# Kernel tuning notes

Measured on AMD Instinct MI355X. Metric: run time of the kernel, lower is better.

The kernel has to match this reference:

```python
import jax, jax.numpy as jnp
import numpy as np

EPS = 1e-12  # torch F.normalize default eps


def _l2_normalize(t):
    n = jnp.linalg.norm(t, axis=-1, keepdims=True)
    return t / jnp.maximum(n, EPS)


def _block(x, W, alpha):
    # x: [B,H,N,D]; W: [D,D] (torch Linear weight, applied as x @ W.T)
    xn = _l2_normalize(x)                                   # q_norm == k_norm (q=k=x)
    A = jnp.einsum('bhnd,bhmd->bhnm', xn, xn)               # cosine similarity [B,H,N,N]
    A = jax.nn.softmax(A / jnp.maximum(alpha, 0.01), axis=-1)
    av = jnp.einsum('bhnm,bhmd->bhnd', A, x)                # A @ v, v = x
    return jax.nn.relu(jnp.einsum('bhnd,ed->bhne', av, W) + x)


def setup_inputs() -> dict:
    key = jax.random.key(0)
    k1, k2, k3 = jax.random.split(key, 3)
    B, H, N, D = 4, 4, 4096, 64
    x = jax.random.normal(k1, (B, H, N, D), dtype=jnp.float32)
    # nn.Linear(dim, dim, bias=False) weights, kaiming-uniform-ish scale
    bound = 1.0 / np.sqrt(D)
    W1 = jax.random.uniform(k2, (D, D), dtype=jnp.float32, minval=-bound, maxval=bound)
    W2 = jax.random.uniform(k3, (D, D), dtype=jnp.float32, minval=-bound, maxval=bound)
    alpha1 = jnp.float32(1.0)
    alpha2 = jnp.float32(1.0)
    return {"x": x, "W1": W1, "W2": W2, "alpha1": alpha1, "alpha2": alpha2}


def reference(x, W1, W2, alpha1, alpha2):
    x = _block(x, W1, alpha1)
    x = _block(x, W2, alpha2)
    return x
```

## Files before the change

kernel.cpp:

```cpp
#include <hip/hip_runtime.h>

typedef unsigned short u16;
typedef unsigned int   u32;
typedef __bf16 bf16x8 __attribute__((ext_vector_type(8)));
typedef float  f32x16 __attribute__((ext_vector_type(16)));

#define BH    16
#define NSEQ  4096
#define DIM   64
#define BM    128
#define BN    64
#define LDP   72
#define NTH   32
#define QTILES (NSEQ / BM)

#define SK_OFF   0
#define SV_OFF   9216
#define SW_OFF   18432
#define LX_OFF   23040
#define SMEM_U16 23552
#define HBUF     4608

__device__ __forceinline__ float bf2f(u16 u) {
    union { u32 i; float f; } v; v.i = ((u32)u) << 16; return v.f;
}
__device__ __forceinline__ u16 f2bf(float f) {
    union { float f; u32 i; } v; v.f = f;
    u32 r = v.i + 0x7fffu + ((v.i >> 16) & 1u);
    return (u16)(r >> 16);
}
#if __has_builtin(__builtin_amdgcn_exp2f)
__device__ __forceinline__ float exp2_raw(float x) { return __builtin_amdgcn_exp2f(x); }
#else
__device__ __forceinline__ float exp2_raw(float x) {
    float r; asm("v_exp_f32 %0, %1" : "=v"(r) : "v"(x)); return r;
}
#endif
__device__ __forceinline__ u32 cvtpk(float a, float b) {
    u32 r; asm("v_cvt_pk_bf16_f32 %0, %1, %2" : "=v"(r) : "v"(a), "v"(b)); return r;
}
__device__ __forceinline__ void plswap(u32& a, u32& b) {
    asm("v_permlane32_swap_b32 %0, %1" : "+v"(a), "+v"(b));
}
__device__ __forceinline__ void lds_barrier() {
    asm volatile("s_waitcnt lgkmcnt(0)\n\ts_barrier" ::: "memory");
}

__global__ __launch_bounds__(256) void ContentGCN_5059471475267_prep(
    const void* __restrict__ src, int isf,
    u16* __restrict__ xn, u16* __restrict__ xT)
{
    __shared__ u16 tile[64 * 72];
    int bh = blockIdx.x >> 6, nt = blockIdx.x & 63, tid = threadIdx.x;
    int r = tid >> 2, cg = (tid & 3) * 16;
    size_t base = ((size_t)bh * NSEQ + nt * 64 + r) * DIM + cg;

    float v[16];
    if (isf) {
        const float4* g = (const float4*)((const float*)src + base);
#pragma unroll
        for (int i = 0; i < 4; i++) {
            float4 t = g[i];
            v[4*i] = t.x; v[4*i+1] = t.y; v[4*i+2] = t.z; v[4*i+3] = t.w;
        }
    } else {
        alignas(16) u16 tmp[16];
        const uint4* g = (const uint4*)((const u16*)src + base);
        ((uint4*)tmp)[0] = g[0]; ((uint4*)tmp)[1] = g[1];
#pragma unroll
        for (int d = 0; d < 16; d++) v[d] = bf2f(tmp[d]);
    }

    float ss = 0.f;
#pragma unroll
    for (int d = 0; d < 16; d++) ss += v[d] * v[d];
    ss += __shfl_xor(ss, 1);
    ss += __shfl_xor(ss, 2);
    float n = sqrtf(ss);
    if (n < 1e-12f) n = 1e-12f;
    float inv = 1.0f / n;

    alignas(16) u16 nb[16], rb[16];
#pragma unroll
    for (int d = 0; d < 16; d++) { nb[d] = f2bf(v[d] * inv); rb[d] = f2bf(v[d]); }
    uint4* gn = (uint4*)(xn + base);
    gn[0] = ((uint4*)nb)[0]; gn[1] = ((uint4*)nb)[1];

    uint4* tr = (uint4*)&tile[r * 72 + cg];
    tr[0] = ((uint4*)rb)[0]; tr[1] = ((uint4*)rb)[1];
    __syncthreads();

    int d = tid >> 2, sc = (tid & 3) * 16;
    alignas(16) u16 ob[16];
#pragma unroll
    for (int j = 0; j < 16; j++) ob[j] = tile[(sc + j) * 72 + d];
    uint4* gt = (uint4*)(xT + ((size_t)bh * DIM + d) * NSEQ + (size_t)nt * 64 + sc);
    gt[0] = ((uint4*)ob)[0]; gt[1] = ((uint4*)ob)[1];
}

__global__ __launch_bounds__(512, 4) void ContentGCN_5059471475267_attn(
    const u16* __restrict__ xn, const u16* __restrict__ xT,
    const void* __restrict__ res, int res_isf,
    const float* __restrict__ Wt, const float* __restrict__ alphap,
    void* __restrict__ outp, int out_isf)
{
    __shared__ u16 smem[SMEM_U16];
    u16* sK = smem + SK_OFF;
    u16* sV = smem + SV_OFF;
    u16* sW = smem + SW_OFF;
    float* lX = (float*)(smem + LX_OFF);

    int tid  = threadIdx.x;
    int w    = tid >> 6, lane = tid & 63;
    int half = w >> 2,  wv   = w & 3;
    int l31  = lane & 31, hi = lane >> 5;
    int bh   = blockIdx.x >> 5;
    int qt   = blockIdx.x & 31;

    float scale = 1.4426950408889634f / fmaxf(alphap[0], 0.01f);

    {
        int rr = tid >> 3, c0 = (tid & 7) * 8;
        const float4* gw = (const float4*)(Wt + rr * DIM + c0);
        float4 t0 = gw[0], t1 = gw[1];
        alignas(16) u16 wb[8];
        wb[0] = f2bf(t0.x); wb[1] = f2bf(t0.y); wb[2] = f2bf(t0.z); wb[3] = f2bf(t0.w);
        wb[4] = f2bf(t1.x); wb[5] = f2bf(t1.y); wb[6] = f2bf(t1.z); wb[7] = f2bf(t1.w);
        *(uint4*)&sW[rr * LDP + c0] = *(const uint4*)wb;
    }

    int qrow = qt * BM + wv * 32 + l31;
    const u16* qp = xn + ((size_t)bh * NSEQ + qrow) * DIM + hi * 8;
    bf16x8 bQ0 = *(const bf16x8*)(qp);
    bf16x8 bQ1 = *(const bf16x8*)(qp + 16);
    bf16x8 bQ2 = *(const bf16x8*)(qp + 32);
    bf16x8 bQ3 = *(const bf16x8*)(qp + 48);

    f32x16 z16;
#pragma unroll
    for (int i = 0; i < 16; i++) z16[i] = 0.f;
    f32x16 OT0 = z16, OT1 = z16;
    float la0 = 0.f, la1 = 0.f, la2 = 0.f, la3 = 0.f;

    u16* sKh = sK + half * HBUF;
    u16* sVh = sV + half * HBUF;

    int ltid = tid & 255;
    int srow = ltid >> 2, scol = (ltid & 3) * 16;

    const u16* pk = xn + ((size_t)bh * NSEQ + half * (NTH * BN) + srow) * DIM + scol;
    const u16* pv = xT + ((size_t)bh * DIM + srow) * NSEQ + half * (NTH * BN) + scol;
    uint4 ck0 = ((const uint4*)pk)[0], ck1 = ((const uint4*)pk)[1];
    uint4 cv0 = ((const uint4*)pv)[0], cv1 = ((const uint4*)pv)[1];
    pk += (size_t)BN * DIM; pv += BN;

    const u16* kB = sKh + l31 * LDP + hi * 8;
    const u16* vB0 = sVh + l31 * LDP + hi * 8;
    const u16* vB1 = sVh + (32 + l31) * LDP + hi * 8;

    for (int kt = 0; kt < NTH; kt++) {
        lds_barrier();
        *(uint4*)&sKh[srow * LDP + scol]     = ck0;
        *(uint4*)&sKh[srow * LDP + scol + 8] = ck1;
        *(uint4*)&sVh[srow * LDP + scol]     = cv0;
        *(uint4*)&sVh[srow * LDP + scol + 8] = cv1;
        if (kt + 1 < NTH) {
            ck0 = ((const uint4*)pk)[0]; ck1 = ((const uint4*)pk)[1];
            cv0 = ((const uint4*)pv)[0]; cv1 = ((const uint4*)pv)[1];
            pk += (size_t)BN * DIM; pv += BN;
        }
        lds_barrier();

#pragma unroll
        for (int kb = 0; kb < 2; kb++) {
            const u16* kb0 = kB + kb * 32 * LDP;
            f32x16 ST;
            ST = __builtin_amdgcn_mfma_f32_32x32x16_bf16(*(const bf16x8*)(kb0),      bQ0, z16, 0, 0, 0);
            ST = __builtin_amdgcn_mfma_f32_32x32x16_bf16(*(const bf16x8*)(kb0 + 16), bQ1, ST,  0, 0, 0);
            ST = __builtin_amdgcn_mfma_f32_32x32x16_bf16(*(const bf16x8*)(kb0 + 32), bQ2, ST,  0, 0, 0);
            ST = __builtin_amdgcn_mfma_f32_32x32x16_bf16(*(const bf16x8*)(kb0 + 48), bQ3, ST,  0, 0, 0);

            float p0  = exp2_raw(fmaf(ST[0],  scale, -scale));
            float p1  = exp2_raw(fmaf(ST[1],  scale, -scale));
            float p2  = exp2_raw(fmaf(ST[2],  scale, -scale));
            float p3  = exp2_raw(fmaf(ST[3],  scale, -scale));
            float p4  = exp2_raw(fmaf(ST[4],  scale, -scale));
            float p5  = exp2_raw(fmaf(ST[5],  scale, -scale));
            float p6  = exp2_raw(fmaf(ST[6],  scale, -scale));
            float p7  = exp2_raw(fmaf(ST[7],  scale, -scale));
            float p8  = exp2_raw(fmaf(ST[8],  scale, -scale));
            float p9  = exp2_raw(fmaf(ST[9],  scale, -scale));
            float p10 = exp2_raw(fmaf(ST[10], scale, -scale));
            float p11 = exp2_raw(fmaf(ST[11], scale, -scale));
            float p12 = exp2_raw(fmaf(ST[12], scale, -scale));
            float p13 = exp2_raw(fmaf(ST[13], scale, -scale));
            float p14 = exp2_raw(fmaf(ST[14], scale, -scale));
            float p15 = exp2_raw(fmaf(ST[15], scale, -scale));

            la0 += (p0 + p4) + (p8  + p12);
            la1 += (p1 + p5) + (p9  + p13);
            la2 += (p2 + p6) + (p10 + p14);
            la3 += (p3 + p7) + (p11 + p15);

            u32 w0 = cvtpk(p0,  p1),  w1 = cvtpk(p2,  p3);
            u32 w2 = cvtpk(p4,  p5),  w3 = cvtpk(p6,  p7);
            u32 w4 = cvtpk(p8,  p9),  w5 = cvtpk(p10, p11);
            u32 w6 = cvtpk(p12, p13), w7 = cvtpk(p14, p15);
            plswap(w0, w2); plswap(w1, w3);
            plswap(w4, w6); plswap(w5, w7);
            union { u32 u[4]; bf16x8 v; } bp0, bp1;
            bp0.u[0] = w0; bp0.u[1] = w1; bp0.u[2] = w2; bp0.u[3] = w3;
            bp1.u[0] = w4; bp1.u[1] = w5; bp1.u[2] = w6; bp1.u[3] = w7;

            const u16* v0 = vB0 + kb * 32;
            const u16* v1 = vB1 + kb * 32;
            OT0 = __builtin_amdgcn_mfma_f32_32x32x16_bf16(*(const bf16x8*)(v0),      bp0.v, OT0, 0, 0, 0);
            OT0 = __builtin_amdgcn_mfma_f32_32x32x16_bf16(*(const bf16x8*)(v0 + 16), bp1.v, OT0, 0, 0, 0);
            OT1 = __builtin_amdgcn_mfma_f32_32x32x16_bf16(*(const bf16x8*)(v1),      bp0.v, OT1, 0, 0, 0);
            OT1 = __builtin_amdgcn_mfma_f32_32x32x16_bf16(*(const bf16x8*)(v1 + 16), bp1.v, OT1, 0, 0, 0);
        }
    }

    float lsum = (la0 + la1) + (la2 + la3);
    u32 ja = __float_as_uint(lsum), jb = ja;
    plswap(ja, jb);
    float lfull = __uint_as_float(ja) + __uint_as_float(jb);

    __syncthreads();
    if (lane < 32) lX[w * 32 + l31] = lfull;
    __syncthreads();
    float invl = 1.0f / (lfull + lX[(w ^ 4) * 32 + l31]);

    union { u32 u[4]; bf16x8 v; } av0, av1, av2, av3;
    {
        u32 x0 = cvtpk(OT0[0]  * invl, OT0[1]  * invl), x1 = cvtpk(OT0[2]  * invl, OT0[3]  * invl);
        u32 x2 = cvtpk(OT0[4]  * invl, OT0[5]  * invl), x3 = cvtpk(OT0[6]  * invl, OT0[7]  * invl);
        u32 x4 = cvtpk(OT0[8]  * invl, OT0[9]  * invl), x5 = cvtpk(OT0[10] * invl, OT0[11] * invl);
        u32 x6 = cvtpk(OT0[12] * invl, OT0[13] * invl), x7 = cvtpk(OT0[14] * invl, OT0[15] * invl);
        plswap(x0, x2); plswap(x1, x3); plswap(x4, x6); plswap(x5, x7);
        av0.u[0] = x0; av0.u[1] = x1; av0.u[2] = x2; av0.u[3] = x3;
        av1.u[0] = x4; av1.u[1] = x5; av1.u[2] = x6; av1.u[3] = x7;
        u32 y0 = cvtpk(OT1[0]  * invl, OT1[1]  * invl), y1 = cvtpk(OT1[2]  * invl, OT1[3]  * invl);
        u32 y2 = cvtpk(OT1[4]  * invl, OT1[5]  * invl), y3 = cvtpk(OT1[6]  * invl, OT1[7]  * invl);
        u32 y4 = cvtpk(OT1[8]  * invl, OT1[9]  * invl), y5 = cvtpk(OT1[10] * invl, OT1[11] * invl);
        u32 y6 = cvtpk(OT1[12] * invl, OT1[13] * invl), y7 = cvtpk(OT1[14] * invl, OT1[15] * invl);
        plswap(y0, y2); plswap(y1, y3); plswap(y4, y6); plswap(y5, y7);
        av2.u[0] = y0; av2.u[1] = y1; av2.u[2] = y2; av2.u[3] = y3;
        av3.u[0] = y4; av3.u[1] = y5; av3.u[2] = y6; av3.u[3] = y7;
    }

    f32x16 R0, R1;
    {
        const u16* w0p = sW + l31 * LDP + hi * 8;
        const u16* w1p = sW + (32 + l31) * LDP + hi * 8;
        R0 = __builtin_amdgcn_mfma_f32_32x32x16_bf16(*(const bf16x8*)(w0p),      av0.v, z16, 0, 0, 0);
        R0 = __builtin_amdgcn_mfma_f32_32x32x16_bf16(*(const bf16x8*)(w0p + 16), av1.v, R0,  0, 0, 0);
        R0 = __builtin_amdgcn_mfma_f32_32x32x16_bf16(*(const bf16x8*)(w0p + 32), av2.v, R0,  0, 0, 0);
        R0 = __builtin_amdgcn_mfma_f32_32x32x16_bf16(*(const bf16x8*)(w0p + 48), av3.v, R0,  0, 0, 0);
        R1 = __builtin_amdgcn_mfma_f32_32x32x16_bf16(*(const bf16x8*)(w1p),      av0.v, z16, 0, 0, 0);
        R1 = __builtin_amdgcn_mfma_f32_32x32x16_bf16(*(const bf16x8*)(w1p + 16), av1.v, R1,  0, 0, 0);
        R1 = __builtin_amdgcn_mfma_f32_32x32x16_bf16(*(const bf16x8*)(w1p + 32), av2.v, R1,  0, 0, 0);
        R1 = __builtin_amdgcn_mfma_f32_32x32x16_bf16(*(const bf16x8*)(w1p + 48), av3.v, R1,  0, 0, 0);
    }

    float* outS = (float*)smem;
    if (half == 0) {
#pragma unroll
        for (int r = 0; r < 16; r++) {
            int e0 = (r & 3) + 8 * (r >> 2) + 4 * hi;
            outS[e0 * 133 + wv * 32 + l31]        = R0[r];
            outS[(e0 + 32) * 133 + wv * 32 + l31] = R1[r];
        }
    }
    __syncthreads();
    if (half == 1) {
#pragma unroll
        for (int r = 0; r < 16; r++) {
            int e0 = (r & 3) + 8 * (r >> 2) + 4 * hi;
            outS[e0 * 133 + wv * 32 + l31]        += R0[r];
            outS[(e0 + 32) * 133 + wv * 32 + l31] += R1[r];
        }
    }
    __syncthreads();

    {
        int q = tid >> 2, c = tid & 3;
        size_t gbase = ((size_t)bh * NSEQ + qt * BM + q) * DIM + c * 16;
        float vv[16];
#pragma unroll
        for (int j = 0; j < 16; j++) vv[j] = outS[(c * 16 + j) * 133 + q];
        if (res_isf) {
            const float4* rp = (const float4*)((const float*)res + gbase);
#pragma unroll
            for (int i = 0; i < 4; i++) {
                float4 t = rp[i];
                vv[4*i] += t.x; vv[4*i+1] += t.y; vv[4*i+2] += t.z; vv[4*i+3] += t.w;
            }
        } else {
            alignas(16) u16 rb[16];
            const uint4* rp = (const uint4*)((const u16*)res + gbase);
            ((uint4*)rb)[0] = rp[0]; ((uint4*)rb)[1] = rp[1];
#pragma unroll
            for (int j = 0; j < 16; j++) vv[j] += bf2f(rb[j]);
        }
#pragma unroll
        for (int j = 0; j < 16; j++) vv[j] = (vv[j] < 0.f) ? 0.f : vv[j];
        if (out_isf) {
            float4* op = (float4*)((float*)outp + gbase);
#pragma unroll
            for (int i = 0; i < 4; i++)
                op[i] = make_float4(vv[4*i], vv[4*i+1], vv[4*i+2], vv[4*i+3]);
        } else {
            alignas(16) u16 ob[16];
#pragma unroll
            for (int j = 0; j < 16; j++) ob[j] = f2bf(vv[j]);
            uint4* op = (uint4*)((u16*)outp + gbase);
            op[0] = ((uint4*)ob)[0]; op[1] = ((uint4*)ob)[1];
        }
    }
}

extern "C" void kernel_launch(void* const* d_in, const int* in_sizes, int n_in,
                              void* d_out, int out_size, void* d_ws, size_t ws_size,
                              hipStream_t stream) {
    const float* x  = (const float*)d_in[0];
    const float* W1 = (const float*)d_in[1];
    const float* W2 = (const float*)d_in[2];
    const float* a1 = (const float*)d_in[3];
    const float* a2 = (const float*)d_in[4];
    float* outp = (float*)d_out;

    size_t elems = (size_t)BH * NSEQ * DIM;
    u16* xn = (u16*)d_ws;
    u16* xT = xn + elems;
    u16* y1 = xT + elems;

    dim3 pgrid(BH * 64),     pblk(256);
    dim3 agrid(BH * QTILES), ablk(512);

    ContentGCN_5059471475267_prep<<<pgrid, pblk, 0, stream>>>(x, 1, xn, xT);
    ContentGCN_5059471475267_attn<<<agrid, ablk, 0, stream>>>(xn, xT, x, 1, W1, a1, y1, 0);
    ContentGCN_5059471475267_prep<<<pgrid, pblk, 0, stream>>>(y1, 0, xn, xT);
    ContentGCN_5059471475267_attn<<<agrid, ablk, 0, stream>>>(xn, xT, y1, 0, W2, a2, outp, 1);
}
```

Baseline: 248.0 us.

## Use LDS transpose reads for V and fuse second-block normalization into attention epilogue

V is now kept row-major (no transposed copy), staged into LDS in a swizzled layout and read with ds_read_b64_tr_b16 so the MFMA operand is transposed on load. The first attention kernel's epilogue now also writes the L2-normalized bf16 output, which removes the second prep launch and its global round trip. This adds inline asm with explicit waitcnt and sched barriers that may limit overlap, and it depends on the transpose-read layout math being correct.

```diff
diff --git a/kernel.cpp b/kernel.cpp
--- a/kernel.cpp
+++ b/kernel.cpp
@@ -4,6 +4,7 @@
 typedef unsigned int   u32;
 typedef __bf16 bf16x8 __attribute__((ext_vector_type(8)));
 typedef float  f32x16 __attribute__((ext_vector_type(16)));
+typedef u32    u32x2  __attribute__((ext_vector_type(2)));
 
 #define BH    16
 #define NSEQ  4096
@@ -16,10 +17,13 @@
 
 #define SK_OFF   0
 #define SV_OFF   9216
-#define SW_OFF   18432
-#define LX_OFF   23040
-#define SMEM_U16 23552
-#define HBUF     4608
+#define SW_OFF   17408
+#define LX_OFF   22016
+#define SMEM_U16 22528
+#define K_HBUF   4608
+#define V_HBUF   4096
+
+#define MFMA __builtin_amdgcn_mfma_f32_32x32x16_bf16
 
 __device__ __forceinline__ float bf2f(u16 u) {
     union { u32 i; float f; } v; v.i = ((u32)u) << 16; return v.f;
@@ -47,28 +51,18 @@
 }
 
 __global__ __launch_bounds__(256) void ContentGCN_5059471475267_prep(
-    const void* __restrict__ src, int isf,
-    u16* __restrict__ xn, u16* __restrict__ xT)
+    const float* __restrict__ src, u16* __restrict__ xn, u16* __restrict__ xr)
 {
-    __shared__ u16 tile[64 * 72];
     int bh = blockIdx.x >> 6, nt = blockIdx.x & 63, tid = threadIdx.x;
     int r = tid >> 2, cg = (tid & 3) * 16;
     size_t base = ((size_t)bh * NSEQ + nt * 64 + r) * DIM + cg;
 
     float v[16];
-    if (isf) {
-        const float4* g = (const float4*)((const float*)src + base);
-#pragma unroll
-        for (int i = 0; i < 4; i++) {
-            float4 t = g[i];
-            v[4*i] = t.x; v[4*i+1] = t.y; v[4*i+2] = t.z; v[4*i+3] = t.w;
-        }
-    } else {
-        alignas(16) u16 tmp[16];
-        const uint4* g = (const uint4*)((const u16*)src + base);
-        ((uint4*)tmp)[0] = g[0]; ((uint4*)tmp)[1] = g[1];
-#pragma unroll
-        for (int d = 0; d < 16; d++) v[d] = bf2f(tmp[d]);
+    const float4* g = (const float4*)(src + base);
+#pragma unroll
+    for (int i = 0; i < 4; i++) {
+        float4 t = g[i];
+        v[4*i] = t.x; v[4*i+1] = t.y; v[4*i+2] = t.z; v[4*i+3] = t.w;
     }
 
     float ss = 0.f;
@@ -85,24 +79,15 @@
     for (int d = 0; d < 16; d++) { nb[d] = f2bf(v[d] * inv); rb[d] = f2bf(v[d]); }
     uint4* gn = (uint4*)(xn + base);
     gn[0] = ((uint4*)nb)[0]; gn[1] = ((uint4*)nb)[1];
-
-    uint4* tr = (uint4*)&tile[r * 72 + cg];
-    tr[0] = ((uint4*)rb)[0]; tr[1] = ((uint4*)rb)[1];
-    __syncthreads();
-
-    int d = tid >> 2, sc = (tid & 3) * 16;
-    alignas(16) u16 ob[16];
-#pragma unroll
-    for (int j = 0; j < 16; j++) ob[j] = tile[(sc + j) * 72 + d];
-    uint4* gt = (uint4*)(xT + ((size_t)bh * DIM + d) * NSEQ + (size_t)nt * 64 + sc);
-    gt[0] = ((uint4*)ob)[0]; gt[1] = ((uint4*)ob)[1];
+    uint4* gr = (uint4*)(xr + base);
+    gr[0] = ((uint4*)rb)[0]; gr[1] = ((uint4*)rb)[1];
 }
 
 __global__ __launch_bounds__(512, 4) void ContentGCN_5059471475267_attn(
-    const u16* __restrict__ xn, const u16* __restrict__ xT,
+    const u16* __restrict__ xn, const u16* __restrict__ xr,
     const void* __restrict__ res, int res_isf,
     const float* __restrict__ Wt, const float* __restrict__ alphap,
-    void* __restrict__ outp, int out_isf)
+    void* __restrict__ outp, int out_isf, u16* __restrict__ xnout)
 {
     __shared__ u16 smem[SMEM_U16];
     u16* sK = smem + SK_OFF;
@@ -142,84 +127,110 @@
     f32x16 OT0 = z16, OT1 = z16;
     float la0 = 0.f, la1 = 0.f, la2 = 0.f, la3 = 0.f;
 
-    u16* sKh = sK + half * HBUF;
-    u16* sVh = sV + half * HBUF;
+    u16* sKh = sK + half * K_HBUF;
+    u16* sVh = sV + half * V_HBUF;
 
     int ltid = tid & 255;
     int srow = ltid >> 2, scol = (ltid & 3) * 16;
+    int vsaddr = ((scol >> 4) * 16 + (srow >> 2)) * 64 + (srow & 3) * 16;
 
     const u16* pk = xn + ((size_t)bh * NSEQ + half * (NTH * BN) + srow) * DIM + scol;
-    const u16* pv = xT + ((size_t)bh * DIM + srow) * NSEQ + half * (NTH * BN) + scol;
+    const u16* pv = xr + ((size_t)bh * NSEQ + half * (NTH * BN) + srow) * DIM + scol;
     uint4 ck0 = ((const uint4*)pk)[0], ck1 = ((const uint4*)pk)[1];
     uint4 cv0 = ((const uint4*)pv)[0], cv1 = ((const uint4*)pv)[1];
-    pk += (size_t)BN * DIM; pv += BN;
+    pk += (size_t)BN * DIM; pv += (size_t)BN * DIM;
 
     const u16* kB = sKh + l31 * LDP + hi * 8;
-    const u16* vB0 = sVh + l31 * LDP + hi * 8;
-    const u16* vB1 = sVh + (32 + l31) * LDP + hi * 8;
+
+    u32 trbase = (u32)(uintptr_t)&sVh[0]
+               + ((u32)((lane >> 4) & 1)) * 2048u
+               + ((u32)hi) * 256u
+               + ((u32)(lane & 15)) * 8u;
+
+#define KBSTEP(KB)                                                              \
+    {                                                                           \
+        const u16* kb0 = kB + (KB) * 32 * LDP;                                  \
+        f32x16 ST;                                                              \
+        ST = MFMA(*(const bf16x8*)(kb0),      bQ0, z16, 0, 0, 0);               \
+        ST = MFMA(*(const bf16x8*)(kb0 + 16), bQ1, ST,  0, 0, 0);               \
+        ST = MFMA(*(const bf16x8*)(kb0 + 32), bQ2, ST,  0, 0, 0);               \
+        ST = MFMA(*(const bf16x8*)(kb0 + 48), bQ3, ST,  0, 0, 0);               \
+        u32x2 t00, t01, t10, t11, t20, t21, t30, t31;                           \
+        asm volatile("ds_read_b64_tr_b16 %0, %1 offset:%2"                      \
+            : "=&v"(t00) : "v"(trbase), "i"((((KB)*8 + 0) * 128)));             \
+        asm volatile("ds_read_b64_tr_b16 %0, %1 offset:%2"                      \
+            : "=&v"(t01) : "v"(trbase), "i"((((KB)*8 + 1) * 128)));             \
+        asm volatile("ds_read_b64_tr_b16 %0, %1 offset:%2"                      \
+            : "=&v"(t10) : "v"(trbase), "i"((((KB)*8 + 4) * 128)));             \
+        asm volatile("ds_read_b64_tr_b16 %0, %1 offset:%2"                      \
+            : "=&v"(t11) : "v"(trbase), "i"((((KB)*8 + 5) * 128)));             \
+        asm volatile("ds_read_b64_tr_b16 %0, %1 offset:%2"                      \
+            : "=&v"(t20) : "v"(trbase), "i"((4096 + ((KB)*8 + 0) * 128)));      \
+        asm volatile("ds_read_b64_tr_b16 %0, %1 offset:%2"                      \
+            : "=&v"(t21) : "v"(trbase), "i"((4096 + ((KB)*8 + 1) * 128)));      \
+        asm volatile("ds_read_b64_tr_b16 %0, %1 offset:%2"                      \
+            : "=&v"(t30) : "v"(trbase), "i"((4096 + ((KB)*8 + 4) * 128)));      \
+        asm volatile("ds_read_b64_tr_b16 %0, %1 offset:%2"                      \
+            : "=&v"(t31) : "v"(trbase), "i"((4096 + ((KB)*8 + 5) * 128)));      \
+        float p0  = exp2_raw(fmaf(ST[0],  scale, -scale));                      \
+        float p1  = exp2_raw(fmaf(ST[1],  scale, -scale));                      \
+        float p2  = exp2_raw(fmaf(ST[2],  scale, -scale));                      \
+        float p3  = exp2_raw(fmaf(ST[3],  scale, -scale));                      \
+        float p4  = exp2_raw(fmaf(ST[4],  scale, -scale));                      \
+        float p5  = exp2_raw(fmaf(ST[5],  scale, -scale));                      \
+        float p6  = exp2_raw(fmaf(ST[6],  scale, -scale));                      \
+        float p7  = exp2_raw(fmaf(ST[7],  scale, -scale));                      \
+        float p8  = exp2_raw(fmaf(ST[8],  scale, -scale));                      \
+        float p9  = exp2_raw(fmaf(ST[9],  scale, -scale));                      \
+        float p10 = exp2_raw(fmaf(ST[10], scale, -scale));                      \
+        float p11 = exp2_raw(fmaf(ST[11], scale, -scale));                      \
+        float p12 = exp2_raw(fmaf(ST[12], scale, -scale));                      \
+        float p13 = exp2_raw(fmaf(ST[13], scale, -scale));                      \
+        float p14 = exp2_raw(fmaf(ST[14], scale, -scale));                      \
+        float p15 = exp2_raw(fmaf(ST[15], scale, -scale));                      \
+        la0 += (p0 + p4) + (p8  + p12);                                         \
+        la1 += (p1 + p5) + (p9  + p13);                                         \
+        la2 += (p2 + p6) + (p10 + p14);                                         \
+        la3 += (p3 + p7) + (p11 + p15);                                         \
+        u32 w0 = cvtpk(p0,  p1),  w1 = cvtpk(p2,  p3);                          \
+        u32 w2 = cvtpk(p4,  p5),  w3 = cvtpk(p6,  p7);                          \
+        u32 w4 = cvtpk(p8,  p9),  w5 = cvtpk(p10, p11);                         \
+        u32 w6 = cvtpk(p12, p13), w7 = cvtpk(p14, p15);                         \
+        plswap(w0, w2); plswap(w1, w3);                                         \
+        plswap(w4, w6); plswap(w5, w7);                                         \
+        union { u32 u[4]; bf16x8 v; } bp0, bp1;                                 \
+        bp0.u[0] = w0; bp0.u[1] = w1; bp0.u[2] = w2; bp0.u[3] = w3;             \
+        bp1.u[0] = w4; bp1.u[1] = w5; bp1.u[2] = w6; bp1.u[3] = w7;             \
+        asm volatile("s_waitcnt lgkmcnt(0)" ::: "memory");                      \
+        __builtin_amdgcn_sched_barrier(0);                                      \
+        union { u32 u[4]; bf16x8 v; } vf00, vf01, vf10, vf11;                   \
+        vf00.u[0] = t00.x; vf00.u[1] = t00.y; vf00.u[2] = t01.x; vf00.u[3] = t01.y; \
+        vf01.u[0] = t10.x; vf01.u[1] = t10.y; vf01.u[2] = t11.x; vf01.u[3] = t11.y; \
+        vf10.u[0] = t20.x; vf10.u[1] = t20.y; vf10.u[2] = t21.x; vf10.u[3] = t21.y; \
+        vf11.u[0] = t30.x; vf11.u[1] = t30.y; vf11.u[2] = t31.x; vf11.u[3] = t31.y; \
+        OT0 = MFMA(vf00.v, bp0.v, OT0, 0, 0, 0);                                \
+        OT0 = MFMA(vf01.v, bp1.v, OT0, 0, 0, 0);                                \
+        OT1 = MFMA(vf10.v, bp0.v, OT1, 0, 0, 0);                                \
+        OT1 = MFMA(vf11.v, bp1.v, OT1, 0, 0, 0);                                \
+    }
 
     for (int kt = 0; kt < NTH; kt++) {
         lds_barrier();
         *(uint4*)&sKh[srow * LDP + scol]     = ck0;
         *(uint4*)&sKh[srow * LDP + scol + 8] = ck1;
-        *(uint4*)&sVh[srow * LDP + scol]     = cv0;
-        *(uint4*)&sVh[srow * LDP + scol + 8] = cv1;
+        *(uint4*)&sVh[vsaddr]     = cv0;
+        *(uint4*)&sVh[vsaddr + 8] = cv1;
         if (kt + 1 < NTH) {
             ck0 = ((const uint4*)pk)[0]; ck1 = ((const uint4*)pk)[1];
             cv0 = ((const uint4*)pv)[0]; cv1 = ((const uint4*)pv)[1];
-            pk += (size_t)BN * DIM; pv += BN;
+            pk += (size_t)BN * DIM; pv += (size_t)BN * DIM;
         }
         lds_barrier();
 
-#pragma unroll
-        for (int kb = 0; kb < 2; kb++) {
-            const u16* kb0 = kB + kb * 32 * LDP;
-            f32x16 ST;
-            ST = __builtin_amdgcn_mfma_f32_32x32x16_bf16(*(const bf16x8*)(kb0),      bQ0, z16, 0, 0, 0);
-            ST = __builtin_amdgcn_mfma_f32_32x32x16_bf16(*(const bf16x8*)(kb0 + 16), bQ1, ST,  0, 0, 0);
-            ST = __builtin_amdgcn_mfma_f32_32x32x16_bf16(*(const bf16x8*)(kb0 + 32), bQ2, ST,  0, 0, 0);
-            ST = __builtin_amdgcn_mfma_f32_32x32x16_bf16(*(const bf16x8*)(kb0 + 48), bQ3, ST,  0, 0, 0);
-
-            float p0  = exp2_raw(fmaf(ST[0],  scale, -scale));
-            float p1  = exp2_raw(fmaf(ST[1],  scale, -scale));
-            float p2  = exp2_raw(fmaf(ST[2],  scale, -scale));
-            float p3  = exp2_raw(fmaf(ST[3],  scale, -scale));
-            float p4  = exp2_raw(fmaf(ST[4],  scale, -scale));
-            float p5  = exp2_raw(fmaf(ST[5],  scale, -scale));
-            float p6  = exp2_raw(fmaf(ST[6],  scale, -scale));
-            float p7  = exp2_raw(fmaf(ST[7],  scale, -scale));
-            float p8  = exp2_raw(fmaf(ST[8],  scale, -scale));
-            float p9  = exp2_raw(fmaf(ST[9],  scale, -scale));
-            float p10 = exp2_raw(fmaf(ST[10], scale, -scale));
-            float p11 = exp2_raw(fmaf(ST[11], scale, -scale));
-            float p12 = exp2_raw(fmaf(ST[12], scale, -scale));
-            float p13 = exp2_raw(fmaf(ST[13], scale, -scale));
-            float p14 = exp2_raw(fmaf(ST[14], scale, -scale));
-            float p15 = exp2_raw(fmaf(ST[15], scale, -scale));
-
-            la0 += (p0 + p4) + (p8  + p12);
-            la1 += (p1 + p5) + (p9  + p13);
-            la2 += (p2 + p6) + (p10 + p14);
-            la3 += (p3 + p7) + (p11 + p15);
-
-            u32 w0 = cvtpk(p0,  p1),  w1 = cvtpk(p2,  p3);
-            u32 w2 = cvtpk(p4,  p5),  w3 = cvtpk(p6,  p7);
-            u32 w4 = cvtpk(p8,  p9),  w5 = cvtpk(p10, p11);
-            u32 w6 = cvtpk(p12, p13), w7 = cvtpk(p14, p15);
-            plswap(w0, w2); plswap(w1, w3);
-            plswap(w4, w6); plswap(w5, w7);
-            union { u32 u[4]; bf16x8 v; } bp0, bp1;
-            bp0.u[0] = w0; bp0.u[1] = w1; bp0.u[2] = w2; bp0.u[3] = w3;
-            bp1.u[0] = w4; bp1.u[1] = w5; bp1.u[2] = w6; bp1.u[3] = w7;
-
-            const u16* v0 = vB0 + kb * 32;
-            const u16* v1 = vB1 + kb * 32;
-            OT0 = __builtin_amdgcn_mfma_f32_32x32x16_bf16(*(const bf16x8*)(v0),      bp0.v, OT0, 0, 0, 0);
-            OT0 = __builtin_amdgcn_mfma_f32_32x32x16_bf16(*(const bf16x8*)(v0 + 16), bp1.v, OT0, 0, 0, 0);
-            OT1 = __builtin_amdgcn_mfma_f32_32x32x16_bf16(*(const bf16x8*)(v1),      bp0.v, OT1, 0, 0, 0);
-            OT1 = __builtin_amdgcn_mfma_f32_32x32x16_bf16(*(const bf16x8*)(v1 + 16), bp1.v, OT1, 0, 0, 0);
-        }
-    }
+        KBSTEP(0)
+        KBSTEP(1)
+    }
+#undef KBSTEP
 
     float lsum = (la0 + la1) + (la2 + la3);
     u32 ja = __float_as_uint(lsum), jb = ja;
@@ -253,14 +264,14 @@
     {
         const u16* w0p = sW + l31 * LDP + hi * 8;
         const u16* w1p = sW + (32 + l31) * LDP + hi * 8;
-        R0 = __builtin_amdgcn_mfma_f32_32x32x16_bf16(*(const bf16x8*)(w0p),      av0.v, z16, 0, 0, 0);
-        R0 = __builtin_amdgcn_mfma_f32_32x32x16_bf16(*(const bf16x8*)(w0p + 16), av1.v, R0,  0, 0, 0);
-        R0 = __builtin_amdgcn_mfma_f32_32x32x16_bf16(*(const bf16x8*)(w0p + 32), av2.v, R0,  0, 0, 0);
-        R0 = __builtin_amdgcn_mfma_f32_32x32x16_bf16(*(const bf16x8*)(w0p + 48), av3.v, R0,  0, 0, 0);
-        R1 = __builtin_amdgcn_mfma_f32_32x32x16_bf16(*(const bf16x8*)(w1p),      av0.v, z16, 0, 0, 0);
-        R1 = __builtin_amdgcn_mfma_f32_32x32x16_bf16(*(const bf16x8*)(w1p + 16), av1.v, R1,  0, 0, 0);
-        R1 = __builtin_amdgcn_mfma_f32_32x32x16_bf16(*(const bf16x8*)(w1p + 32), av2.v, R1,  0, 0, 0);
-        R1 = __builtin_amdgcn_mfma_f32_32x32x16_bf16(*(const bf16x8*)(w1p + 48), av3.v, R1,  0, 0, 0);
+        R0 = MFMA(*(const bf16x8*)(w0p),      av0.v, z16, 0, 0, 0);
+        R0 = MFMA(*(const bf16x8*)(w0p + 16), av1.v, R0,  0, 0, 0);
+        R0 = MFMA(*(const bf16x8*)(w0p + 32), av2.v, R0,  0, 0, 0);
+        R0 = MFMA(*(const bf16x8*)(w0p + 48), av3.v, R0,  0, 0, 0);
+        R1 = MFMA(*(const bf16x8*)(w1p),      av0.v, z16, 0, 0, 0);
+        R1 = MFMA(*(const bf16x8*)(w1p + 16), av1.v, R1,  0, 0, 0);
+        R1 = MFMA(*(const bf16x8*)(w1p + 32), av2.v, R1,  0, 0, 0);
+        R1 = MFMA(*(const bf16x8*)(w1p + 48), av3.v, R1,  0, 0, 0);
     }
 
     float* outS = (float*)smem;
@@ -316,6 +327,21 @@
             for (int j = 0; j < 16; j++) ob[j] = f2bf(vv[j]);
             uint4* op = (uint4*)((u16*)outp + gbase);
             op[0] = ((uint4*)ob)[0]; op[1] = ((uint4*)ob)[1];
+        }
+        if (xnout) {
+            float ss = 0.f;
+#pragma unroll
+            for (int j = 0; j < 16; j++) ss += vv[j] * vv[j];
+            ss += __shfl_xor(ss, 1);
+            ss += __shfl_xor(ss, 2);
+            float n = sqrtf(ss);
+            if (n < 1e-12f) n = 1e-12f;
+            float inv = 1.0f / n;
+            alignas(16) u16 nb[16];
+#pragma unroll
+            for (int j = 0; j < 16; j++) nb[j] = f2bf(vv[j] * inv);
+            uint4* gn = (uint4*)(xnout + gbase);
+            gn[0] = ((uint4*)nb)[0]; gn[1] = ((uint4*)nb)[1];
         }
     }
 }
@@ -331,15 +357,17 @@
     float* outp = (float*)d_out;
 
     size_t elems = (size_t)BH * NSEQ * DIM;
-    u16* xn = (u16*)d_ws;
-    u16* xT = xn + elems;
-    u16* y1 = xT + elems;
+    u16* xn1 = (u16*)d_ws;
+    u16* xr1 = xn1 + elems;
+    u16* xn2 = xr1 + elems;
+    u16* xr2 = xn2 + elems;
 
     dim3 pgrid(BH * 64),     pblk(256);
     dim3 agrid(BH * QTILES), ablk(512);
 
-    ContentGCN_5059471475267_prep<<<pgrid, pblk, 0, stream>>>(x, 1, xn, xT);
-    ContentGCN_5059471475267_attn<<<agrid, ablk, 0, stream>>>(xn, xT, x, 1, W1, a1, y1, 0);
-    ContentGCN_5059471475267_prep<<<pgrid, pblk, 0, stream>>>(y1, 0, xn, xT);
-    ContentGCN_5059471475267_attn<<<agrid, ablk, 0, stream>>>(xn, xT, y1, 0, W2, a2, outp, 1);
-}
+    ContentGCN_5059471475267_prep<<<pgrid, pblk, 0, stream>>>(x, xn1, xr1);
+    ContentGCN_5059471475267_attn<<<agrid, ablk, 0, stream>>>(
+        xn1, xr1, x, 1, W1, a1, xr2, 0, xn2);
+    ContentGCN_5059471475267_attn<<<agrid, ablk, 0, stream>>>(
+        xn2, xr2, xr2, 0, W2, a2, outp, 1, nullptr);
+}
```

Result: slower. 272.7 us (+9.9%).

## Fuse second-block normalization into attn epilogue and restructure QK/PV MFMA schedule

Applied to the files above, without the earlier changes.

The first attention kernel's epilogue now also L2-normalizes its output rows and writes them as bf16 to a new buffer. The second prep pass therefore only has to transpose y1, and the prep kernels now give each thread a full row, with 256 rows per block. The inner loop issues both QK^T MFMA chains before the exp/PV work and wraps the MFMA groups in s_setprio so matrix work can overlap with the exp computation. The cost is higher register pressure (64-float rows in prep, two score accumulators in attn) and extra epilogue work in the attention kernel.

```diff
diff --git a/kernel.cpp b/kernel.cpp
--- a/kernel.cpp
+++ b/kernel.cpp
@@ -21,6 +21,8 @@
 #define SMEM_U16 23552
 #define HBUF     4608
 
+#define MFMA __builtin_amdgcn_mfma_f32_32x32x16_bf16
+
 __device__ __forceinline__ float bf2f(u16 u) {
     union { u32 i; float f; } v; v.i = ((u32)u) << 16; return v.f;
 }
@@ -47,62 +49,75 @@
 }
 
 __global__ __launch_bounds__(256) void ContentGCN_5059471475267_prep(
-    const void* __restrict__ src, int isf,
-    u16* __restrict__ xn, u16* __restrict__ xT)
+    const float* __restrict__ src, u16* __restrict__ xn, u16* __restrict__ xT)
 {
-    __shared__ u16 tile[64 * 72];
-    int bh = blockIdx.x >> 6, nt = blockIdx.x & 63, tid = threadIdx.x;
-    int r = tid >> 2, cg = (tid & 3) * 16;
-    size_t base = ((size_t)bh * NSEQ + nt * 64 + r) * DIM + cg;
-
-    float v[16];
-    if (isf) {
-        const float4* g = (const float4*)((const float*)src + base);
-#pragma unroll
-        for (int i = 0; i < 4; i++) {
-            float4 t = g[i];
-            v[4*i] = t.x; v[4*i+1] = t.y; v[4*i+2] = t.z; v[4*i+3] = t.w;
-        }
-    } else {
-        alignas(16) u16 tmp[16];
-        const uint4* g = (const uint4*)((const u16*)src + base);
-        ((uint4*)tmp)[0] = g[0]; ((uint4*)tmp)[1] = g[1];
-#pragma unroll
-        for (int d = 0; d < 16; d++) v[d] = bf2f(tmp[d]);
+    __shared__ u16 tile[256 * 72];
+    int bh = blockIdx.x >> 4, nt = blockIdx.x & 15, tid = threadIdx.x;
+    size_t base = ((size_t)bh * NSEQ + nt * 256 + tid) * DIM;
+
+    float v[64];
+    const float4* g = (const float4*)(src + base);
+#pragma unroll
+    for (int i = 0; i < 16; i++) {
+        float4 t4 = g[i];
+        v[4*i] = t4.x; v[4*i+1] = t4.y; v[4*i+2] = t4.z; v[4*i+3] = t4.w;
     }
 
     float ss = 0.f;
 #pragma unroll
-    for (int d = 0; d < 16; d++) ss += v[d] * v[d];
-    ss += __shfl_xor(ss, 1);
-    ss += __shfl_xor(ss, 2);
+    for (int d = 0; d < 64; d++) ss += v[d] * v[d];
     float n = sqrtf(ss);
     if (n < 1e-12f) n = 1e-12f;
     float inv = 1.0f / n;
 
-    alignas(16) u16 nb[16], rb[16];
-#pragma unroll
-    for (int d = 0; d < 16; d++) { nb[d] = f2bf(v[d] * inv); rb[d] = f2bf(v[d]); }
+    alignas(16) u16 nb[64], rb[64];
+#pragma unroll
+    for (int d = 0; d < 64; d++) { nb[d] = f2bf(v[d] * inv); rb[d] = f2bf(v[d]); }
     uint4* gn = (uint4*)(xn + base);
-    gn[0] = ((uint4*)nb)[0]; gn[1] = ((uint4*)nb)[1];
-
-    uint4* tr = (uint4*)&tile[r * 72 + cg];
-    tr[0] = ((uint4*)rb)[0]; tr[1] = ((uint4*)rb)[1];
-    __syncthreads();
-
-    int d = tid >> 2, sc = (tid & 3) * 16;
-    alignas(16) u16 ob[16];
-#pragma unroll
-    for (int j = 0; j < 16; j++) ob[j] = tile[(sc + j) * 72 + d];
-    uint4* gt = (uint4*)(xT + ((size_t)bh * DIM + d) * NSEQ + (size_t)nt * 64 + sc);
-    gt[0] = ((uint4*)ob)[0]; gt[1] = ((uint4*)ob)[1];
+#pragma unroll
+    for (int i = 0; i < 8; i++) gn[i] = ((uint4*)nb)[i];
+
+    uint4* trow = (uint4*)&tile[tid * 72];
+#pragma unroll
+    for (int i = 0; i < 8; i++) trow[i] = ((uint4*)rb)[i];
+    __syncthreads();
+
+    int d = tid & 63, ch = tid >> 6;
+    alignas(16) u16 ob[64];
+#pragma unroll
+    for (int nn = 0; nn < 64; nn++) ob[nn] = tile[(ch * 64 + nn) * 72 + d];
+    uint4* gt = (uint4*)(xT + ((size_t)bh * DIM + d) * NSEQ + (size_t)nt * 256 + ch * 64);
+#pragma unroll
+    for (int i = 0; i < 8; i++) gt[i] = ((uint4*)ob)[i];
+}
+
+__global__ __launch_bounds__(256) void ContentGCN_5059471475267_prept(
+    const u16* __restrict__ src, u16* __restrict__ xT)
+{
+    __shared__ u16 tile[256 * 72];
+    int bh = blockIdx.x >> 4, nt = blockIdx.x & 15, tid = threadIdx.x;
+    size_t base = ((size_t)bh * NSEQ + nt * 256 + tid) * DIM;
+
+    uint4* trow = (uint4*)&tile[tid * 72];
+    const uint4* g = (const uint4*)(src + base);
+#pragma unroll
+    for (int i = 0; i < 8; i++) trow[i] = g[i];
+    __syncthreads();
+
+    int d = tid & 63, ch = tid >> 6;
+    alignas(16) u16 ob[64];
+#pragma unroll
+    for (int nn = 0; nn < 64; nn++) ob[nn] = tile[(ch * 64 + nn) * 72 + d];
+    uint4* gt = (uint4*)(xT + ((size_t)bh * DIM + d) * NSEQ + (size_t)nt * 256 + ch * 64);
+#pragma unroll
+    for (int i = 0; i < 8; i++) gt[i] = ((uint4*)ob)[i];
 }
 
 __global__ __launch_bounds__(512, 4) void ContentGCN_5059471475267_attn(
     const u16* __restrict__ xn, const u16* __restrict__ xT,
     const void* __restrict__ res, int res_isf,
     const float* __restrict__ Wt, const float* __restrict__ alphap,
-    void* __restrict__ outp, int out_isf)
+    void* __restrict__ outp, int out_isf, u16* __restrict__ xnout)
 {
     __shared__ u16 smem[SMEM_U16];
     u16* sK = smem + SK_OFF;
@@ -154,7 +169,7 @@
     uint4 cv0 = ((const uint4*)pv)[0], cv1 = ((const uint4*)pv)[1];
     pk += (size_t)BN * DIM; pv += BN;
 
-    const u16* kB = sKh + l31 * LDP + hi * 8;
+    const u16* kB  = sKh + l31 * LDP + hi * 8;
     const u16* vB0 = sVh + l31 * LDP + hi * 8;
     const u16* vB1 = sVh + (32 + l31) * LDP + hi * 8;
 
@@ -171,37 +186,36 @@
         }
         lds_barrier();
 
-#pragma unroll
-        for (int kb = 0; kb < 2; kb++) {
-            const u16* kb0 = kB + kb * 32 * LDP;
-            f32x16 ST;
-            ST = __builtin_amdgcn_mfma_f32_32x32x16_bf16(*(const bf16x8*)(kb0),      bQ0, z16, 0, 0, 0);
-            ST = __builtin_amdgcn_mfma_f32_32x32x16_bf16(*(const bf16x8*)(kb0 + 16), bQ1, ST,  0, 0, 0);
-            ST = __builtin_amdgcn_mfma_f32_32x32x16_bf16(*(const bf16x8*)(kb0 + 32), bQ2, ST,  0, 0, 0);
-            ST = __builtin_amdgcn_mfma_f32_32x32x16_bf16(*(const bf16x8*)(kb0 + 48), bQ3, ST,  0, 0, 0);
-
-            float p0  = exp2_raw(fmaf(ST[0],  scale, -scale));
-            float p1  = exp2_raw(fmaf(ST[1],  scale, -scale));
-            float p2  = exp2_raw(fmaf(ST[2],  scale, -scale));
-            float p3  = exp2_raw(fmaf(ST[3],  scale, -scale));
-            float p4  = exp2_raw(fmaf(ST[4],  scale, -scale));
-            float p5  = exp2_raw(fmaf(ST[5],  scale, -scale));
-            float p6  = exp2_raw(fmaf(ST[6],  scale, -scale));
-            float p7  = exp2_raw(fmaf(ST[7],  scale, -scale));
-            float p8  = exp2_raw(fmaf(ST[8],  scale, -scale));
-            float p9  = exp2_raw(fmaf(ST[9],  scale, -scale));
-            float p10 = exp2_raw(fmaf(ST[10], scale, -scale));
-            float p11 = exp2_raw(fmaf(ST[11], scale, -scale));
-            float p12 = exp2_raw(fmaf(ST[12], scale, -scale));
-            float p13 = exp2_raw(fmaf(ST[13], scale, -scale));
-            float p14 = exp2_raw(fmaf(ST[14], scale, -scale));
-            float p15 = exp2_raw(fmaf(ST[15], scale, -scale));
-
-            la0 += (p0 + p4) + (p8  + p12);
-            la1 += (p1 + p5) + (p9  + p13);
-            la2 += (p2 + p6) + (p10 + p14);
-            la3 += (p3 + p7) + (p11 + p15);
-
+        const u16* kb1 = kB + 32 * LDP;
+        f32x16 ST0, ST1;
+        __builtin_amdgcn_s_setprio(1);
+        ST0 = MFMA(*(const bf16x8*)(kB),       bQ0, z16, 0, 0, 0);
+        ST0 = MFMA(*(const bf16x8*)(kB + 16),  bQ1, ST0, 0, 0, 0);
+        ST0 = MFMA(*(const bf16x8*)(kB + 32),  bQ2, ST0, 0, 0, 0);
+        ST0 = MFMA(*(const bf16x8*)(kB + 48),  bQ3, ST0, 0, 0, 0);
+        ST1 = MFMA(*(const bf16x8*)(kb1),      bQ0, z16, 0, 0, 0);
+        ST1 = MFMA(*(const bf16x8*)(kb1 + 16), bQ1, ST1, 0, 0, 0);
+        ST1 = MFMA(*(const bf16x8*)(kb1 + 32), bQ2, ST1, 0, 0, 0);
+        ST1 = MFMA(*(const bf16x8*)(kb1 + 48), bQ3, ST1, 0, 0, 0);
+        __builtin_amdgcn_s_setprio(0);
+
+        {
+            float p0  = exp2_raw(fmaf(ST0[0],  scale, -scale));
+            float p1  = exp2_raw(fmaf(ST0[1],  scale, -scale));
+            float p2  = exp2_raw(fmaf(ST0[2],  scale, -scale));
+            float p3  = exp2_raw(fmaf(ST0[3],  scale, -scale));
+            float p4  = exp2_raw(fmaf(ST0[4],  scale, -scale));
+            float p5  = exp2_raw(fmaf(ST0[5],  scale, -scale));
+            float p6  = exp2_raw(fmaf(ST0[6],  scale, -scale));
+            float p7  = exp2_raw(fmaf(ST0[7],  scale, -scale));
+            float p8  = exp2_raw(fmaf(ST0[8],  scale, -scale));
+            float p9  = exp2_raw(fmaf(ST0[9],  scale, -scale));
+            float p10 = exp2_raw(fmaf(ST0[10], scale, -scale));
+            float p11 = exp2_raw(fmaf(ST0[11], scale, -scale));
+            float p12 = exp2_raw(fmaf(ST0[12], scale, -scale));
+            float p13 = exp2_raw(fmaf(ST0[13], scale, -scale));
+            float p14 = exp2_raw(fmaf(ST0[14], scale, -scale));
+            float p15 = exp2_raw(fmaf(ST0[15], scale, -scale));
             u32 w0 = cvtpk(p0,  p1),  w1 = cvtpk(p2,  p3);
             u32 w2 = cvtpk(p4,  p5),  w3 = cvtpk(p6,  p7);
             u32 w4 = cvtpk(p8,  p9),  w5 = cvtpk(p10, p11);
@@ -211,13 +225,54 @@
             union { u32 u[4]; bf16x8 v; } bp0, bp1;
             bp0.u[0] = w0; bp0.u[1] = w1; bp0.u[2] = w2; bp0.u[3] = w3;
             bp1.u[0] = w4; bp1.u[1] = w5; bp1.u[2] = w6; bp1.u[3] = w7;
-
-            const u16* v0 = vB0 + kb * 32;
-            const u16* v1 = vB1 + kb * 32;
-            OT0 = __builtin_amdgcn_mfma_f32_32x32x16_bf16(*(const bf16x8*)(v0),      bp0.v, OT0, 0, 0, 0);
-            OT0 = __builtin_amdgcn_mfma_f32_32x32x16_bf16(*(const bf16x8*)(v0 + 16), bp1.v, OT0, 0, 0, 0);
-            OT1 = __builtin_amdgcn_mfma_f32_32x32x16_bf16(*(const bf16x8*)(v1),      bp0.v, OT1, 0, 0, 0);
-            OT1 = __builtin_amdgcn_mfma_f32_32x32x16_bf16(*(const bf16x8*)(v1 + 16), bp1.v, OT1, 0, 0, 0);
+            __builtin_amdgcn_s_setprio(1);
+            OT0 = MFMA(*(const bf16x8*)(vB0),      bp0.v, OT0, 0, 0, 0);
+            OT0 = MFMA(*(const bf16x8*)(vB0 + 16), bp1.v, OT0, 0, 0, 0);
+            OT1 = MFMA(*(const bf16x8*)(vB1),      bp0.v, OT1, 0, 0, 0);
+            OT1 = MFMA(*(const bf16x8*)(vB1 + 16), bp1.v, OT1, 0, 0, 0);
+            __builtin_amdgcn_s_setprio(0);
+            la0 += (p0 + p4) + (p8  + p12);
+            la1 += (p1 + p5) + (p9  + p13);
+            la2 += (p2 + p6) + (p10 + p14);
+            la3 += (p3 + p7) + (p11 + p15);
+        }
+
+        {
+            float p0  = exp2_raw(fmaf(ST1[0],  scale, -scale));
+            float p1  = exp2_raw(fmaf(ST1[1],  scale, -scale));
+            float p2  = exp2_raw(fmaf(ST1[2],  scale, -scale));
+            float p3  = exp2_raw(fmaf(ST1[3],  scale, -scale));
+            float p4  = exp2_raw(fmaf(ST1[4],  scale, -scale));
+            float p5  = exp2_raw(fmaf(ST1[5],  scale, -scale));
+            float p6  = exp2_raw(fmaf(ST1[6],  scale, -scale));
+            float p7  = exp2_raw(fmaf(ST1[7],  scale, -scale));
+            float p8  = exp2_raw(fmaf(ST1[8],  scale, -scale));
+            float p9  = exp2_raw(fmaf(ST1[9],  scale, -scale));
+            float p10 = exp2_raw(fmaf(ST1[10], scale, -scale));
+            float p11 = exp2_raw(fmaf(ST1[11], scale, -scale));
+            float p12 = exp2_raw(fmaf(ST1[12], scale, -scale));
+            float p13 = exp2_raw(fmaf(ST1[13], scale, -scale));
+            float p14 = exp2_raw(fmaf(ST1[14], scale, -scale));
+            float p15 = exp2_raw(fmaf(ST1[15], scale, -scale));
+            u32 w0 = cvtpk(p0,  p1),  w1 = cvtpk(p2,  p3);
+            u32 w2 = cvtpk(p4,  p5),  w3 = cvtpk(p6,  p7);
+            u32 w4 = cvtpk(p8,  p9),  w5 = cvtpk(p10, p11);
+            u32 w6 = cvtpk(p12, p13), w7 = cvtpk(p14, p15);
+            plswap(w0, w2); plswap(w1, w3);
+            plswap(w4, w6); plswap(w5, w7);
+            union { u32 u[4]; bf16x8 v; } bp0, bp1;
+            bp0.u[0] = w0; bp0.u[1] = w1; bp0.u[2] = w2; bp0.u[3] = w3;
+            bp1.u[0] = w4; bp1.u[1] = w5; bp1.u[2] = w6; bp1.u[3] = w7;
+            __builtin_amdgcn_s_setprio(1);
+            OT0 = MFMA(*(const bf16x8*)(vB0 + 32), bp0.v, OT0, 0, 0, 0);
+            OT0 = MFMA(*(const bf16x8*)(vB0 + 48), bp1.v, OT0, 0, 0, 0);
+            OT1 = MFMA(*(const bf16x8*)(vB1 + 32), bp0.v, OT1, 0, 0, 0);
+            OT1 = MFMA(*(const bf16x8*)(vB1 + 48), bp1.v, OT1, 0, 0, 0);
+            __builtin_amdgcn_s_setprio(0);
+            la0 += (p0 + p4) + (p8  + p12);
+            la1 += (p1 + p5) + (p9  + p13);
+            la2 += (p2 + p6) + (p10 + p14);
+            la3 += (p3 + p7) + (p11 + p15);
         }
     }
 
@@ -253,14 +308,14 @@
     {
         const u16* w0p = sW + l31 * LDP + hi * 8;
         const u16* w1p = sW + (32 + l31) * LDP + hi * 8;
-        R0 = __builtin_amdgcn_mfma_f32_32x32x16_bf16(*(const bf16x8*)(w0p),      av0.v, z16, 0, 0, 0);
-        R0 = __builtin_amdgcn_mfma_f32_32x32x16_bf16(*(const bf16x8*)(w0p + 16), av1.v, R0,  0, 0, 0);
-        R0 = __builtin_amdgcn_mfma_f32_32x32x16_bf16(*(const bf16x8*)(w0p + 32), av2.v, R0,  0, 0, 0);
-        R0 = __builtin_amdgcn_mfma_f32_32x32x16_bf16(*(const bf16x8*)(w0p + 48), av3.v, R0,  0, 0, 0);
-        R1 = __builtin_amdgcn_mfma_f32_32x32x16_bf16(*(const bf16x8*)(w1p),      av0.v, z16, 0, 0, 0);
-        R1 = __builtin_amdgcn_mfma_f32_32x32x16_bf16(*(const bf16x8*)(w1p + 16), av1.v, R1,  0, 0, 0);
-        R1 = __builtin_amdgcn_mfma_f32_32x32x16_bf16(*(const bf16x8*)(w1p + 32), av2.v, R1,  0, 0, 0);
-        R1 = __builtin_amdgcn_mfma_f32_32x32x16_bf16(*(const bf16x8*)(w1p + 48), av3.v, R1,  0, 0, 0);
+        R0 = MFMA(*(const bf16x8*)(w0p),      av0.v, z16, 0, 0, 0);
+        R0 = MFMA(*(const bf16x8*)(w0p + 16), av1.v, R0,  0, 0, 0);
+        R0 = MFMA(*(const bf16x8*)(w0p + 32), av2.v, R0,  0, 0, 0);
+        R0 = MFMA(*(const bf16x8*)(w0p + 48), av3.v, R0,  0, 0, 0);
+        R1 = MFMA(*(const bf16x8*)(w1p),      av0.v, z16, 0, 0, 0);
+        R1 = MFMA(*(const bf16x8*)(w1p + 16), av1.v, R1,  0, 0, 0);
+        R1 = MFMA(*(const bf16x8*)(w1p + 32), av2.v, R1,  0, 0, 0);
+        R1 = MFMA(*(const bf16x8*)(w1p + 48), av3.v, R1,  0, 0, 0);
     }
 
     float* outS = (float*)smem;
@@ -316,6 +371,21 @@
             for (int j = 0; j < 16; j++) ob[j] = f2bf(vv[j]);
             uint4* op = (uint4*)((u16*)outp + gbase);
             op[0] = ((uint4*)ob)[0]; op[1] = ((uint4*)ob)[1];
+        }
+        if (xnout) {
+            float ss = 0.f;
+#pragma unroll
+            for (int j = 0; j < 16; j++) ss += vv[j] * vv[j];
+            ss += __shfl_xor(ss, 1);
+            ss += __shfl_xor(ss, 2);
+            float n = sqrtf(ss);
+            if (n < 1e-12f) n = 1e-12f;
+            float inv = 1.0f / n;
+            alignas(16) u16 nb[16];
+#pragma unroll
+            for (int j = 0; j < 16; j++) nb[j] = f2bf(vv[j] * inv);
+            uint4* gn = (uint4*)(xnout + gbase);
+            gn[0] = ((uint4*)nb)[0]; gn[1] = ((uint4*)nb)[1];
         }
     }
 }
@@ -331,15 +401,18 @@
     float* outp = (float*)d_out;
 
     size_t elems = (size_t)BH * NSEQ * DIM;
-    u16* xn = (u16*)d_ws;
-    u16* xT = xn + elems;
-    u16* y1 = xT + elems;
-
-    dim3 pgrid(BH * 64),     pblk(256);
+    u16* xn1 = (u16*)d_ws;
+    u16* xT  = xn1 + elems;
+    u16* xn2 = xT + elems;
+    u16* y1  = xn2 + elems;
+
+    dim3 pgrid(BH * 16),     pblk(256);
     dim3 agrid(BH * QTILES), ablk(512);
 
-    ContentGCN_5059471475267_prep<<<pgrid, pblk, 0, stream>>>(x, 1, xn, xT);
-    ContentGCN_5059471475267_attn<<<agrid, ablk, 0, stream>>>(xn, xT, x, 1, W1, a1, y1, 0);
-    ContentGCN_5059471475267_prep<<<pgrid, pblk, 0, stream>>>(y1, 0, xn, xT);
-    ContentGCN_5059471475267_attn<<<agrid, ablk, 0, stream>>>(xn, xT, y1, 0, W2, a2, outp, 1);
-}
+    ContentGCN_5059471475267_prep<<<pgrid, pblk, 0, stream>>>(x, xn1, xT);
+    ContentGCN_5059471475267_attn<<<agrid, ablk, 0, stream>>>(
+        xn1, xT, x, 1, W1, a1, y1, 0, xn2);
+    ContentGCN_5059471475267_prept<<<pgrid, pblk, 0, stream>>>(y1, xT);
+    ContentGCN_5059471475267_attn<<<agrid, ablk, 0, stream>>>(
+        xn2, xT, y1, 0, W2, a2, outp, 1, nullptr);
+}
```

Measured after the change: 246.5 us. About the same (-0.6%).
